# Kernel tuning notes

Measured on AMD Instinct MI355X. Metric: run time of the kernel, lower is better.

## Reference

```python
import jax, jax.numpy as jnp
import numpy as np

R = 16       # voxel resolution
CH = 64      # channels
NSAMPLE = 16
PROJ = 3


def _bn(x, p, eps):
    # p: [4, C] rows = (gamma, beta, running_mean, running_var); eval-mode BN
    g, b, m, v = p
    sh = [1] * x.ndim
    sh[1] = -1
    return (x - m.reshape(sh)) * (g.reshape(sh) * jax.lax.rsqrt(v.reshape(sh) + eps)) + b.reshape(sh)


def _gather_ch(x, flat_idx):
    # x: [B, C, M], flat_idx: [B, L] -> [B, C, L]
    B, C, _ = x.shape
    idx = jnp.broadcast_to(flat_idx[:, None, :], (B, C, flat_idx.shape[1]))
    return jnp.take_along_axis(x, idx, axis=2)


def _pvb_forward(x, xyz, idx, w3d1, b3d1, bn3d1, w3d2, b3d2, bn3d2, proj_w1, proj_bn, proj_w2, pt_bn):
    B, C, N = x.shape
    r = R
    # ---------- voxelization (coords detached, normalize=False) ----------
    nc = xyz - xyz.mean(axis=2, keepdims=True)
    nc = jnp.clip((nc + 1.0) * 0.5 * r, 0.0, r - 1.0)
    nc = jax.lax.stop_gradient(nc)                        # [B,3,N] float in [0, r-1]
    vi = jnp.round(nc).astype(jnp.int32)
    flat = (vi[:, 0] * r + vi[:, 1]) * r + vi[:, 2]       # [B,N]
    seg = (flat + jnp.arange(B, dtype=jnp.int32)[:, None] * (r ** 3)).reshape(-1)
    feats = x.transpose(0, 2, 1).reshape(B * N, C)
    sums = jax.ops.segment_sum(feats, seg, num_segments=B * r ** 3)
    cnts = jax.ops.segment_sum(jnp.ones((B * N,), x.dtype), seg, num_segments=B * r ** 3)
    v = (sums / jnp.maximum(cnts, 1.0)[:, None]).reshape(B, r, r, r, C).transpose(0, 4, 1, 2, 3)
    # ---------- depthwise Conv3d -> BN3d -> LeakyReLU (x2) ----------
    dn = ('NCDHW', 'OIDHW', 'NCDHW')
    v = jax.lax.conv_general_dilated(v, w3d1, (1, 1, 1), 'SAME', dimension_numbers=dn,
                                     feature_group_count=C) + b3d1.reshape(1, C, 1, 1, 1)
    v = jax.nn.leaky_relu(_bn(v, bn3d1, 1e-4), 0.1)
    v = jax.lax.conv_general_dilated(v, w3d2, (1, 1, 1), 'SAME', dimension_numbers=dn,
                                     feature_group_count=C) + b3d2.reshape(1, C, 1, 1, 1)
    v = jax.nn.leaky_relu(_bn(v, bn3d2, 1e-4), 0.1)
    # ---------- trilinear devoxelize ----------
    vf = v.reshape(B, C, r ** 3)
    lo = jnp.floor(nc).astype(jnp.int32)
    fr = nc - lo
    hi = jnp.minimum(lo + 1, r - 1)
    p_v_x = jnp.zeros((B, C, N), x.dtype)
    for dx in (0, 1):
        for dy in (0, 1):
            for dz in (0, 1):
                xi = hi[:, 0] if dx else lo[:, 0]
                yi = hi[:, 1] if dy else lo[:, 1]
                zi = hi[:, 2] if dz else lo[:, 2]
                w = ((fr[:, 0] if dx else 1.0 - fr[:, 0]) *
                     (fr[:, 1] if dy else 1.0 - fr[:, 1]) *
                     (fr[:, 2] if dz else 1.0 - fr[:, 2]))
                p_v_x = p_v_x + w[:, None, :] * _gather_ch(vf, (xi * r + yi) * r + zi)
    # ---------- neighbor gather (precomputed ball-query idx) ----------
    K = idx.shape[-1]
    flat_nb = idx.reshape(B, N * K)
    x_j = _gather_ch(x, flat_nb).reshape(B, C, N, K)
    xyz_j = _gather_ch(xyz, flat_nb).reshape(B, 3, N, K)
    dp1 = xyz_j - xyz[:, :, :, None]                      # [B,3,N,K]
    df = x_j - x[:, :, :, None]                           # [B,C,N,K]
    # proj_conv: 1x1 conv -> BN2d -> ReLU -> 1x1 conv
    h = jnp.einsum('oc,bcnk->bonk', proj_w1, df)
    h = jax.nn.relu(_bn(h, proj_bn, 1e-5))
    dp2 = jnp.einsum('oc,bcnk->bonk', proj_w2, h)         # [B,3,N,K]
    dp = jnp.concatenate([dp1, dp2], axis=1)              # [B,6,N,K]
    # repeat_interleave of the 6 channels up to C (last gets remainder)
    part = 6
    rep = C // part
    repeats = np.array([rep] * (part - 1) + [C - rep * (part - 1)])
    w = jnp.repeat(dp, repeats, axis=1, total_repeat_length=C)
    x_j = x_j * w
    x_j = jax.nn.relu(_bn(x_j, pt_bn, 1e-5))              # proj_transform
    p_p_x = x_j.max(axis=-1)                              # max-pool over neighbors
    return p_v_x + p_p_x                                  # agg_way == 'add'


def setup_inputs() -> dict:
    key = jax.random.key(0)
    ks = jax.random.split(key, 16)
    B, C, N, K = 4, CH, 16384, NSAMPLE

    def bn_params(k, c):
        k1, k2, k3, k4 = jax.random.split(k, 4)
        return jnp.stack([1.0 + 0.1 * jax.random.normal(k1, (c,), jnp.float32),
                          0.1 * jax.random.normal(k2, (c,), jnp.float32),
                          0.1 * jax.random.normal(k3, (c,), jnp.float32),
                          jax.random.uniform(k4, (c,), jnp.float32, 0.5, 1.5)])

    return dict(
        x=jax.random.normal(ks[0], (B, C, N), jnp.float32),
        xyz=jax.random.uniform(ks[1], (B, 3, N), jnp.float32, -1.0, 1.0),
        idx=jax.random.randint(ks[2], (B, N, K), 0, N, jnp.int32),
        w3d1=0.1 * jax.random.normal(ks[3], (C, 1, 3, 3, 3), jnp.float32),
        b3d1=0.01 * jax.random.normal(ks[4], (C,), jnp.float32),
        bn3d1=bn_params(ks[5], C),
        w3d2=0.1 * jax.random.normal(ks[6], (C, 1, 3, 3, 3), jnp.float32),
        b3d2=0.01 * jax.random.normal(ks[7], (C,), jnp.float32),
        bn3d2=bn_params(ks[8], C),
        proj_w1=0.1 * jax.random.normal(ks[9], (PROJ, C), jnp.float32),
        proj_bn=bn_params(ks[10], PROJ),
        proj_w2=0.3 * jax.random.normal(ks[11], (PROJ, PROJ), jnp.float32),
        pt_bn=bn_params(ks[12], C),
    )


def reference(x, xyz, idx, w3d1, b3d1, bn3d1, w3d2, b3d2, bn3d2, proj_w1, proj_bn, proj_w2, pt_bn):
    return _pvb_forward(x, xyz, idx, w3d1, b3d1, bn3d1, w3d2, b3d2, bn3d2, proj_w1, proj_bn, proj_w2, pt_bn)
```

## Files before the change

### kernel.cpp

```cpp
#include <hip/hip_runtime.h>

namespace {
constexpr int B_  = 4;
constexpr int C_  = 64;
constexpr int N_  = 16384;
constexpr int K_  = 16;
constexpr int R3_ = 4096;

constexpr int OFF_MEANS = 0;
constexpr int OFF_XT    = 16;
constexpr int OFF_PTS   = OFF_XT  + B_*N_*C_/2;
constexpr int OFF_SUMS  = OFF_PTS + B_*N_*8;
constexpr int OFF_CNTS  = OFF_SUMS + B_*R3_*C_;
constexpr int OFF_VOX2  = OFF_CNTS + B_*R3_;
}

__device__ __forceinline__ unsigned short f2bf(float f) {
  unsigned u = __float_as_uint(f);
  return (unsigned short)((u + 0x7FFFu + ((u >> 16) & 1u)) >> 16);
}
__device__ __forceinline__ float bf2f(unsigned short h) {
  return __uint_as_float(((unsigned)h) << 16);
}
__device__ __forceinline__ unsigned cvtpk_bf16(float lo, float hi) {
  unsigned r;
  asm("v_cvt_pk_bf16_f32 %0, %1, %2" : "=v"(r) : "v"(lo), "v"(hi));
  return r;
}

__global__ void k_means(const float* __restrict__ xyz, float* __restrict__ means) {
  __shared__ double red[256];
  int blk = blockIdx.x;
  const float* p = xyz + blk * N_;
  double s = 0.0;
  for (int i = threadIdx.x; i < N_; i += 256) s += (double)p[i];
  red[threadIdx.x] = s;
  __syncthreads();
  for (int st = 128; st; st >>= 1) {
    if (threadIdx.x < st) red[threadIdx.x] += red[threadIdx.x + st];
    __syncthreads();
  }
  if (threadIdx.x == 0) means[blk] = (float)(red[0] * (1.0 / (double)N_));
}

__global__ __launch_bounds__(256) void k_prep(
    const float* __restrict__ x, const float* __restrict__ xyz,
    const float* __restrict__ pw1, const float* __restrict__ means,
    unsigned short* __restrict__ xT, float* __restrict__ pts,
    float* __restrict__ sums, float* __restrict__ cnts) {
  __shared__ float tile[64 * 65];
  __shared__ float ncs[3][64];
  __shared__ int   flats[64];

  const int t   = threadIdx.x;
  const int blk = blockIdx.x;
  const int b   = blk >> 8;
  const int n0  = (blk & 255) << 6;

#pragma unroll
  for (int i = 0; i < 16; ++i) {
    int c = i * 4 + (t >> 6);
    int j = t & 63;
    tile[c * 65 + j] = x[((size_t)(b * C_ + c)) * N_ + n0 + j];
  }
  __syncthreads();

#pragma unroll
  for (int i = 0; i < 16; ++i) {
    int p = i * 4 + (t >> 6);
    int c = t & 63;
    xT[((size_t)(b * N_ + n0 + p)) * C_ + c] = f2bf(tile[c * 65 + p]);
  }

  if (t < 192) {
    int p = t & 63, q = t >> 6;
    float s = 0.f;
#pragma unroll
    for (int c = 0; c < 64; ++c) s = fmaf(pw1[q * 64 + c], tile[c * 65 + p], s);
    size_t pb = ((size_t)(b * N_ + n0 + p)) * 8;
    pts[pb + 3 + q] = s;
    float v = xyz[((size_t)(b * 3 + q)) * N_ + n0 + p];
    pts[pb + q] = v;
    float nc = fminf(fmaxf((v - means[b * 3 + q] + 1.0f) * 8.0f, 0.0f), 15.0f);
    ncs[q][p] = nc;
  } else {
    int p = t & 63;
    size_t pb = ((size_t)(b * N_ + n0 + p)) * 8;
    pts[pb + 6] = 0.f;
    pts[pb + 7] = 0.f;
  }
  __syncthreads();

  if (t < 64) {
    int vx = (int)rintf(ncs[0][t]);
    int vy = (int)rintf(ncs[1][t]);
    int vz = (int)rintf(ncs[2][t]);
    int f = (vx * 16 + vy) * 16 + vz;
    flats[t] = f;
    atomicAdd(&cnts[b * R3_ + f], 1.0f);
  }
  __syncthreads();

  const int w = t >> 6, lane = t & 63;
#pragma unroll
  for (int i = 0; i < 16; ++i) {
    int p = w * 16 + i;
    int f = flats[p];
    atomicAdd(&sums[((size_t)(b * R3_ + f)) * C_ + lane], tile[lane * 65 + p]);
  }
}

__global__ __launch_bounds__(256) void k_conv(
    const float* __restrict__ sums, const float* __restrict__ cnts,
    const float* __restrict__ w3d1, const float* __restrict__ b3d1,
    const float* __restrict__ bn1, const float* __restrict__ w3d2,
    const float* __restrict__ b3d2, const float* __restrict__ bn2,
    unsigned short* __restrict__ vox2) {
  __shared__ float va[18 * 18 * 18];
  __shared__ float vb[18 * 18 * 18];
  const int t = threadIdx.x;
  const int b = blockIdx.x >> 6;
  const int c = blockIdx.x & 63;

  float W1[27], W2[27];
#pragma unroll
  for (int i = 0; i < 27; ++i) { W1[i] = w3d1[c * 27 + i]; W2[i] = w3d2[c * 27 + i]; }
  float s1 = bn1[c] / sqrtf(bn1[192 + c] + 1e-4f);
  float d1 = (b3d1[c] - bn1[128 + c]) * s1 + bn1[64 + c];
  float s2 = bn2[c] / sqrtf(bn2[192 + c] + 1e-4f);
  float d2 = (b3d2[c] - bn2[128 + c]) * s2 + bn2[64 + c];

  for (int i = t; i < 18 * 18 * 18; i += 256) { va[i] = 0.f; vb[i] = 0.f; }
  __syncthreads();

#pragma unroll
  for (int i = 0; i < 16; ++i) {
    int vox = t + i * 256;
    int z = vox & 15, y = (vox >> 4) & 15, xx = vox >> 8;
    float cnt = cnts[b * R3_ + vox];
    float v = sums[((size_t)(b * R3_ + vox)) * C_ + c] / fmaxf(cnt, 1.0f);
    va[((xx + 1) * 18 + (y + 1)) * 18 + (z + 1)] = v;
  }
  __syncthreads();

#pragma unroll
  for (int i = 0; i < 16; ++i) {
    int vox = t + i * 256;
    int z = vox & 15, y = (vox >> 4) & 15, xx = vox >> 8;
    int base = ((xx + 1) * 18 + (y + 1)) * 18 + (z + 1);
    float acc = 0.f;
#pragma unroll
    for (int dx = -1; dx <= 1; ++dx)
#pragma unroll
      for (int dy = -1; dy <= 1; ++dy)
#pragma unroll
        for (int dz = -1; dz <= 1; ++dz)
          acc = fmaf(W1[((dx + 1) * 3 + (dy + 1)) * 3 + (dz + 1)],
                     va[base + dx * 324 + dy * 18 + dz], acc);
    float tt = acc * s1 + d1;
    vb[base] = tt > 0.f ? tt : 0.1f * tt;
  }
  __syncthreads();

#pragma unroll
  for (int i = 0; i < 16; ++i) {
    int vox = t + i * 256;
    int z = vox & 15, y = (vox >> 4) & 15, xx = vox >> 8;
    int base = ((xx + 1) * 18 + (y + 1)) * 18 + (z + 1);
    float acc = 0.f;
#pragma unroll
    for (int dx = -1; dx <= 1; ++dx)
#pragma unroll
      for (int dy = -1; dy <= 1; ++dy)
#pragma unroll
        for (int dz = -1; dz <= 1; ++dz)
          acc = fmaf(W2[((dx + 1) * 3 + (dy + 1)) * 3 + (dz + 1)],
                     vb[base + dx * 324 + dy * 18 + dz], acc);
    float tt = acc * s2 + d2;
    vox2[((size_t)(b * R3_ + vox)) * C_ + c] = f2bf(tt > 0.f ? tt : 0.1f * tt);
  }
}

__global__ __launch_bounds__(256, 8) void k_final(
    const unsigned short* __restrict__ xT, const float* __restrict__ pts,
    const unsigned short* __restrict__ vox2, const int* __restrict__ idx,
    const float* __restrict__ means, const float* __restrict__ pbn,
    const float* __restrict__ pw2, const float* __restrict__ ptbn,
    float* __restrict__ out) {
  __shared__ unsigned w6[3][513];
  __shared__ int      jarr[512];
  __shared__ unsigned dv[32][8];
  __shared__ float    outT[64 * 33];

  const int t = threadIdx.x;
  const int blk = blockIdx.x;
  const int xcd = blk & 7;
  const int b = xcd >> 1;
  const int t32 = ((blk >> 3) << 1) | (xcd & 1);
  const int n0 = t32 * 32;

  const float psc0 = pbn[0] * rsqrtf(pbn[9]  + 1e-5f);
  const float psc1 = pbn[1] * rsqrtf(pbn[10] + 1e-5f);
  const float psc2 = pbn[2] * rsqrtf(pbn[11] + 1e-5f);
  const float pof0 = pbn[3] - pbn[6] * psc0;
  const float pof1 = pbn[4] - pbn[7] * psc1;
  const float pof2 = pbn[5] - pbn[8] * psc2;
  float W2r[9];
#pragma unroll
  for (int i = 0; i < 9; ++i) W2r[i] = pw2[i];

  const float* __restrict__ ptsb = pts + (size_t)b * N_ * 8;

#pragma unroll
  for (int rep = 0; rep < 2; ++rep) {
    const int q = t + rep * 256;
    const int p = q >> 4;
    const int n = n0 + p;
    const int j = idx[(size_t)b * N_ * K_ + (size_t)n0 * K_ + q];
    jarr[q] = j;
    const float* qr = ptsb + (size_t)j * 8;
    float4 qa = *(const float4*)qr;
    float4 qb = *(const float4*)(qr + 4);
    const float* ir = ptsb + (size_t)n * 8;
    float4 pa = *(const float4*)ir;
    float4 pb = *(const float4*)(ir + 4);
    float d0 = qa.x - pa.x, d1 = qa.y - pa.y, d2 = qa.z - pa.z;
    float c0 = pof0 - psc0 * pa.w;
    float c1 = pof1 - psc1 * pb.x;
    float c2 = pof2 - psc2 * pb.y;
    float h0 = fmaxf(fmaf(qa.w, psc0, c0), 0.f);
    float h1 = fmaxf(fmaf(qb.x, psc1, c1), 0.f);
    float h2 = fmaxf(fmaf(qb.y, psc2, c2), 0.f);
    float e0 = fmaf(W2r[0], h0, fmaf(W2r[1], h1, W2r[2] * h2));
    float e1 = fmaf(W2r[3], h0, fmaf(W2r[4], h1, W2r[5] * h2));
    float e2 = fmaf(W2r[6], h0, fmaf(W2r[7], h1, W2r[8] * h2));
    w6[0][q] = cvtpk_bf16(d0, d1);
    w6[1][q] = cvtpk_bf16(d2, e0);
    w6[2][q] = cvtpk_bf16(e1, e2);
  }

  if (t < 32) {
    const int n = n0 + t;
    const float* ir = ptsb + (size_t)n * 8;
    float x0 = ir[0], x1 = ir[1], x2 = ir[2];
    float nc0 = fminf(fmaxf((x0 - means[b * 3 + 0] + 1.0f) * 8.0f, 0.0f), 15.0f);
    float nc1 = fminf(fmaxf((x1 - means[b * 3 + 1] + 1.0f) * 8.0f, 0.0f), 15.0f);
    float nc2 = fminf(fmaxf((x2 - means[b * 3 + 2] + 1.0f) * 8.0f, 0.0f), 15.0f);
    int lx = (int)nc0, ly = (int)nc1, lz = (int)nc2;
    float fx = nc0 - (float)lx, fy = nc1 - (float)ly, fz = nc2 - (float)lz;
    int hx = lx < 15 ? lx + 1 : 15;
    int hy = ly < 15 ? ly + 1 : 15;
    int hz = lz < 15 ? lz + 1 : 15;
    float wx[2] = {1.f - fx, fx};
    float wy[2] = {1.f - fy, fy};
    float wz[2] = {1.f - fz, fz};
    int xi[2] = {lx, hx}, yi[2] = {ly, hy}, zi[2] = {lz, hz};
#pragma unroll
    for (int c8 = 0; c8 < 8; ++c8) {
      int dx = c8 >> 2, dy = (c8 >> 1) & 1, dz = c8 & 1;
      int flat = (xi[dx] * 16 + yi[dy]) * 16 + zi[dz];
      float wt = wx[dx] * wy[dy] * wz[dz];
      dv[t][c8] = ((unsigned)flat << 16) | (unsigned)f2bf(wt);
    }
  }
  __syncthreads();

  const int w = t >> 6, lane = t & 63;
  const int widx = lane < 20 ? 0 : lane < 40 ? 1 : 2;
  const bool hi = (lane >= 10 && lane < 20) || (lane >= 30 && lane < 40) || (lane >= 50);
  const float ts = ptbn[lane] * rsqrtf(ptbn[192 + lane] + 1e-5f);
  const float td = ptbn[64 + lane] - ptbn[128 + lane] * ts;
  const unsigned short* __restrict__ xTb = xT + (size_t)b * N_ * C_;
  const unsigned short* __restrict__ voxb = vox2 + (size_t)b * R3_ * C_;

#pragma unroll
  for (int i = 0; i < 8; ++i) {
    const int p = i * 4 + w;

    float acc = 0.f;
#pragma unroll
    for (int c8 = 0; c8 < 8; ++c8) {
      unsigned dvv = dv[p][c8];
      float wt = __uint_as_float(dvv << 16);
      acc = fmaf(wt, bf2f(voxb[(size_t)(dvv >> 16) * C_ + lane]), acc);
    }

    float pm = 0.f;
    const unsigned* w6p = &w6[widx][p * 16];
#pragma unroll
    for (int k = 0; k < 16; ++k) {
      const int j = jarr[p * 16 + k];
      const unsigned short xj = xTb[(size_t)j * C_ + lane];
      const unsigned wvp = w6p[k];
      float wf = hi ? __uint_as_float(wvp & 0xffff0000u)
                    : __uint_as_float(wvp << 16);
      float v = bf2f(xj) * wf;
      pm = fmaxf(pm, fmaf(v, ts, td));
    }

    outT[lane * 33 + p] = acc + pm;
  }
  __syncthreads();

#pragma unroll
  for (int i = 0; i < 8; ++i) {
    int c = i * 8 + (t >> 5);
    int col = t & 31;
    out[((size_t)(b * C_ + c)) * N_ + n0 + col] = outT[c * 33 + col];
  }
}

extern "C" void kernel_launch(void* const* d_in, const int* in_sizes, int n_in,
                              void* d_out, int out_size, void* d_ws, size_t ws_size,
                              hipStream_t stream) {
  const float* x     = (const float*)d_in[0];
  const float* xyz   = (const float*)d_in[1];
  const int*   idx   = (const int*)  d_in[2];
  const float* w3d1  = (const float*)d_in[3];
  const float* b3d1  = (const float*)d_in[4];
  const float* bn3d1 = (const float*)d_in[5];
  const float* w3d2  = (const float*)d_in[6];
  const float* b3d2  = (const float*)d_in[7];
  const float* bn3d2 = (const float*)d_in[8];
  const float* pw1   = (const float*)d_in[9];
  const float* pbn   = (const float*)d_in[10];
  const float* pw2   = (const float*)d_in[11];
  const float* ptbn  = (const float*)d_in[12];
  float* out = (float*)d_out;
  float* ws  = (float*)d_ws;

  hipMemsetAsync(ws + OFF_SUMS, 0, (size_t)(B_ * R3_ * C_ + B_ * R3_) * sizeof(float), stream);

  k_means<<<dim3(12), dim3(256), 0, stream>>>(xyz, ws + OFF_MEANS);
  k_prep<<<dim3(B_ * N_ / 64), dim3(256), 0, stream>>>(
      x, xyz, pw1, ws + OFF_MEANS, (unsigned short*)(ws + OFF_XT), ws + OFF_PTS,
      ws + OFF_SUMS, ws + OFF_CNTS);
  k_conv<<<dim3(B_ * C_), dim3(256), 0, stream>>>(
      ws + OFF_SUMS, ws + OFF_CNTS, w3d1, b3d1, bn3d1, w3d2, b3d2, bn3d2,
      (unsigned short*)(ws + OFF_VOX2));
  k_final<<<dim3(B_ * N_ / 32), dim3(256), 0, stream>>>(
      (const unsigned short*)(ws + OFF_XT), ws + OFF_PTS,
      (const unsigned short*)(ws + OFF_VOX2), idx, ws + OFF_MEANS,
      pbn, pw2, ptbn, out);
}
```

Baseline: 97.94 us.

## Fuse voxel scatter into conv kernel using per-block LDS atomics

Removes the global atomic scatter of per-voxel sums and counts and the workspace memset. Each (batch, channel) conv block now rebuilds its own voxel grid in shared memory by streaming all points, using LDS atomics. This drops contended global atomics and a kernel-boundary round trip. In exchange every block recomputes the voxel index for all points and rereads xyz once per channel, and the per-point data in k_prep is now written with vectorized float4 stores.

New measurement: 117.4 us. 1.2x slower.

```diff
diff --git a/kernel.cpp b/kernel.cpp
--- a/kernel.cpp
+++ b/kernel.cpp
@@ -10,9 +10,7 @@
 constexpr int OFF_MEANS = 0;
 constexpr int OFF_XT    = 16;
 constexpr int OFF_PTS   = OFF_XT  + B_*N_*C_/2;
-constexpr int OFF_SUMS  = OFF_PTS + B_*N_*8;
-constexpr int OFF_CNTS  = OFF_SUMS + B_*R3_*C_;
-constexpr int OFF_VOX2  = OFF_CNTS + B_*R3_;
+constexpr int OFF_VOX2  = OFF_PTS + B_*N_*8;
 }
 
 __device__ __forceinline__ unsigned short f2bf(float f) {
@@ -28,9 +26,10 @@
   return r;
 }
 
-__global__ void k_means(const float* __restrict__ xyz, float* __restrict__ means) {
+__global__ __launch_bounds__(256) void k_init(
+    const float* __restrict__ xyz, float* __restrict__ means) {
   __shared__ double red[256];
-  int blk = blockIdx.x;
+  const int blk = blockIdx.x;
   const float* p = xyz + blk * N_;
   double s = 0.0;
   for (int i = threadIdx.x; i < N_; i += 256) s += (double)p[i];
@@ -45,12 +44,11 @@
 
 __global__ __launch_bounds__(256) void k_prep(
     const float* __restrict__ x, const float* __restrict__ xyz,
-    const float* __restrict__ pw1, const float* __restrict__ means,
-    unsigned short* __restrict__ xT, float* __restrict__ pts,
-    float* __restrict__ sums, float* __restrict__ cnts) {
+    const float* __restrict__ pw1,
+    unsigned short* __restrict__ xT, float* __restrict__ pts) {
   __shared__ float tile[64 * 65];
-  __shared__ float ncs[3][64];
-  __shared__ int   flats[64];
+  __shared__ float xyzs[3][64];
+  __shared__ float hp[3][64];
 
   const int t   = threadIdx.x;
   const int blk = blockIdx.x;
@@ -63,6 +61,10 @@
     int j = t & 63;
     tile[c * 65 + j] = x[((size_t)(b * C_ + c)) * N_ + n0 + j];
   }
+  if (t < 192) {
+    int p = t & 63, q = t >> 6;
+    xyzs[q][p] = xyz[((size_t)(b * 3 + q)) * N_ + n0 + p];
+  }
   __syncthreads();
 
 #pragma unroll
@@ -77,69 +79,73 @@
     float s = 0.f;
 #pragma unroll
     for (int c = 0; c < 64; ++c) s = fmaf(pw1[q * 64 + c], tile[c * 65 + p], s);
-    size_t pb = ((size_t)(b * N_ + n0 + p)) * 8;
-    pts[pb + 3 + q] = s;
-    float v = xyz[((size_t)(b * 3 + q)) * N_ + n0 + p];
-    pts[pb + q] = v;
-    float nc = fminf(fmaxf((v - means[b * 3 + q] + 1.0f) * 8.0f, 0.0f), 15.0f);
-    ncs[q][p] = nc;
-  } else {
-    int p = t & 63;
-    size_t pb = ((size_t)(b * N_ + n0 + p)) * 8;
-    pts[pb + 6] = 0.f;
-    pts[pb + 7] = 0.f;
-  }
-  __syncthreads();
-
-  if (t < 64) {
-    int vx = (int)rintf(ncs[0][t]);
-    int vy = (int)rintf(ncs[1][t]);
-    int vz = (int)rintf(ncs[2][t]);
-    int f = (vx * 16 + vy) * 16 + vz;
-    flats[t] = f;
-    atomicAdd(&cnts[b * R3_ + f], 1.0f);
-  }
-  __syncthreads();
-
-  const int w = t >> 6, lane = t & 63;
-#pragma unroll
-  for (int i = 0; i < 16; ++i) {
-    int p = w * 16 + i;
-    int f = flats[p];
-    atomicAdd(&sums[((size_t)(b * R3_ + f)) * C_ + lane], tile[lane * 65 + p]);
-  }
-}
-
-__global__ __launch_bounds__(256) void k_conv(
-    const float* __restrict__ sums, const float* __restrict__ cnts,
+    hp[q][p] = s;
+  }
+  __syncthreads();
+
+  if (t < 128) {
+    const int p = t >> 1;
+    float4 v;
+    if (t & 1) v = make_float4(hp[1][p], hp[2][p], 0.f, 0.f);
+    else       v = make_float4(xyzs[0][p], xyzs[1][p], xyzs[2][p], hp[0][p]);
+    *(float4*)(pts + ((size_t)(b * N_ + n0 + p)) * 8 + (t & 1) * 4) = v;
+  }
+}
+
+__global__ __launch_bounds__(256) void k_voxconv(
+    const float* __restrict__ x, const float* __restrict__ xyz,
+    const float* __restrict__ means,
     const float* __restrict__ w3d1, const float* __restrict__ b3d1,
     const float* __restrict__ bn1, const float* __restrict__ w3d2,
     const float* __restrict__ b3d2, const float* __restrict__ bn2,
     unsigned short* __restrict__ vox2) {
+  __shared__ float cnt_s[R3_];
+  __shared__ float sum_s[R3_];
   __shared__ float va[18 * 18 * 18];
   __shared__ float vb[18 * 18 * 18];
   const int t = threadIdx.x;
   const int b = blockIdx.x >> 6;
   const int c = blockIdx.x & 63;
 
+#pragma unroll
+  for (int i = 0; i < 16; ++i) { cnt_s[t + i * 256] = 0.f; sum_s[t + i * 256] = 0.f; }
+  for (int i = t; i < 18 * 18 * 18; i += 256) { va[i] = 0.f; vb[i] = 0.f; }
+
   float W1[27], W2[27];
 #pragma unroll
   for (int i = 0; i < 27; ++i) { W1[i] = w3d1[c * 27 + i]; W2[i] = w3d2[c * 27 + i]; }
-  float s1 = bn1[c] / sqrtf(bn1[192 + c] + 1e-4f);
-  float d1 = (b3d1[c] - bn1[128 + c]) * s1 + bn1[64 + c];
-  float s2 = bn2[c] / sqrtf(bn2[192 + c] + 1e-4f);
-  float d2 = (b3d2[c] - bn2[128 + c]) * s2 + bn2[64 + c];
-
-  for (int i = t; i < 18 * 18 * 18; i += 256) { va[i] = 0.f; vb[i] = 0.f; }
+  const float s1 = bn1[c] / sqrtf(bn1[192 + c] + 1e-4f);
+  const float d1 = (b3d1[c] - bn1[128 + c]) * s1 + bn1[64 + c];
+  const float s2 = bn2[c] / sqrtf(bn2[192 + c] + 1e-4f);
+  const float d2 = (b3d2[c] - bn2[128 + c]) * s2 + bn2[64 + c];
+
+  const float m0 = means[b * 3 + 0], m1 = means[b * 3 + 1], m2 = means[b * 3 + 2];
+  const float* __restrict__ xr  = x   + ((size_t)(b * C_ + c)) * N_;
+  const float* __restrict__ xy0 = xyz + ((size_t)(b * 3 + 0)) * N_;
+  const float* __restrict__ xy1 = xyz + ((size_t)(b * 3 + 1)) * N_;
+  const float* __restrict__ xy2 = xyz + ((size_t)(b * 3 + 2)) * N_;
+  __syncthreads();
+
+#pragma unroll 4
+  for (int i = 0; i < 64; ++i) {
+    const int n = t + i * 256;
+    const float xv = xr[n];
+    const float a0 = xy0[n], a1 = xy1[n], a2 = xy2[n];
+    const int vx = (int)rintf(fminf(fmaxf((a0 - m0 + 1.0f) * 8.0f, 0.0f), 15.0f));
+    const int vy = (int)rintf(fminf(fmaxf((a1 - m1 + 1.0f) * 8.0f, 0.0f), 15.0f));
+    const int vz = (int)rintf(fminf(fmaxf((a2 - m2 + 1.0f) * 8.0f, 0.0f), 15.0f));
+    const int f = (vx * 16 + vy) * 16 + vz;
+    atomicAdd(&cnt_s[f], 1.0f);
+    atomicAdd(&sum_s[f], xv);
+  }
   __syncthreads();
 
 #pragma unroll
   for (int i = 0; i < 16; ++i) {
     int vox = t + i * 256;
     int z = vox & 15, y = (vox >> 4) & 15, xx = vox >> 8;
-    float cnt = cnts[b * R3_ + vox];
-    float v = sums[((size_t)(b * R3_ + vox)) * C_ + c] / fmaxf(cnt, 1.0f);
-    va[((xx + 1) * 18 + (y + 1)) * 18 + (z + 1)] = v;
+    va[((xx + 1) * 18 + (y + 1)) * 18 + (z + 1)] =
+        sum_s[vox] / fmaxf(cnt_s[vox], 1.0f);
   }
   __syncthreads();
 
@@ -329,14 +335,11 @@
   float* out = (float*)d_out;
   float* ws  = (float*)d_ws;
 
-  hipMemsetAsync(ws + OFF_SUMS, 0, (size_t)(B_ * R3_ * C_ + B_ * R3_) * sizeof(float), stream);
-
-  k_means<<<dim3(12), dim3(256), 0, stream>>>(xyz, ws + OFF_MEANS);
+  k_init<<<dim3(12), dim3(256), 0, stream>>>(xyz, ws + OFF_MEANS);
   k_prep<<<dim3(B_ * N_ / 64), dim3(256), 0, stream>>>(
-      x, xyz, pw1, ws + OFF_MEANS, (unsigned short*)(ws + OFF_XT), ws + OFF_PTS,
-      ws + OFF_SUMS, ws + OFF_CNTS);
-  k_conv<<<dim3(B_ * C_), dim3(256), 0, stream>>>(
-      ws + OFF_SUMS, ws + OFF_CNTS, w3d1, b3d1, bn3d1, w3d2, b3d2, bn3d2,
+      x, xyz, pw1, (unsigned short*)(ws + OFF_XT), ws + OFF_PTS);
+  k_voxconv<<<dim3(B_ * C_), dim3(256), 0, stream>>>(
+      x, xyz, ws + OFF_MEANS, w3d1, b3d1, bn3d1, w3d2, b3d2, bn3d2,
       (unsigned short*)(ws + OFF_VOX2));
   k_final<<<dim3(B_ * N_ / 32), dim3(256), 0, stream>>>(
       (const unsigned short*)(ws + OFF_XT), ws + OFF_PTS,
```
